# Kernel tuning notes

Measured on AMD Instinct MI355X. Metric: run time of the kernel, lower is better.

## Reference

```python
import jax, jax.numpy as jnp
import numpy as np

NUM_CAPSULE = 32
DIM_VECTOR = 16
NUM_ROUTING = 3

def squash(v, axis=-1):
    s2 = jnp.sum(jnp.square(v), axis=axis, keepdims=True)
    scale = s2 / (1.0 + s2) / jnp.sqrt(s2)
    return scale * v

def setup_inputs() -> dict:
    key = jax.random.key(0)
    k1, k2 = jax.random.split(key)
    B, IN_CAPS, IN_DIM = 64, 2048, 8
    x = jax.random.normal(k1, (B, IN_CAPS, IN_DIM), dtype=jnp.float32)
    # glorot-uniform-ish weight: [in_caps, num_caps, in_dim, out_dim]
    limit = np.sqrt(6.0 / (IN_DIM + DIM_VECTOR)).astype(np.float32)
    W = jax.random.uniform(k2, (IN_CAPS, NUM_CAPSULE, IN_DIM, DIM_VECTOR), dtype=jnp.float32, minval=-limit, maxval=limit)
    return {"x": x, "W": W}

def reference(x, W):
    # x: [B, in_caps, in_dim]; W: [in_caps, num_caps, in_dim, out_dim]
    # inputs_hat (u_hat): [B, in_caps, num_caps, out_dim]
    u_hat = jnp.einsum('bid,inde->bine', x, W)
    B, IN_CAPS = u_hat.shape[0], u_hat.shape[1]
    # routing logits; original broadcasts over out_dim with identical values,
    # so a trailing singleton dim is mathematically equivalent
    b = jnp.zeros((B, IN_CAPS, NUM_CAPSULE, 1), dtype=u_hat.dtype)
    v = None
    for i in range(NUM_ROUTING):
        c = jax.nn.softmax(b, axis=2)                       # over num_capsule
        s = jnp.sum(c * u_hat, axis=1, keepdims=True)       # [B,1,nc,out]
        v = squash(s)                                       # [B,1,nc,out]
        if i != NUM_ROUTING - 1:
            b = b + jnp.sum(u_hat * v, axis=-1, keepdims=True)
    return v.reshape(-1, NUM_CAPSULE, DIM_VECTOR)
```

## Files before the change

kernel.cpp:

```cpp
#include <hip/hip_runtime.h>
#include <math.h>


#define B_TOT 64
#define I_TOT 2048
#define D_IN  8
#define NC    32
#define EV    16
#define OD    (NC*EV)
#define BC    8
#define NBC   (B_TOT/BC)
#define ICH   16
#define NIC   (I_TOT/ICH)

__device__ __forceinline__ void fma4(float4& acc, float a, const float4& w) {
    acc.x = fmaf(a, w.x, acc.x);
    acc.y = fmaf(a, w.y, acc.y);
    acc.z = fmaf(a, w.z, acc.z);
    acc.w = fmaf(a, w.w, acc.w);
}

template <int MODE>
__global__ __launch_bounds__(256, 4)
void route_pass(const float* __restrict__ x, const float* __restrict__ W,
                float* __restrict__ P, const float* __restrict__ vin,
                float* __restrict__ aws)
{
    __shared__ __align__(16) float xl[BC * ICH * D_IN];
    __shared__ float wsum[2][4][BC];

    const int t  = threadIdx.x;
    const int ic = blockIdx.x & (NIC - 1);
    const int bc = blockIdx.x >> 7;
    const int b0 = bc * BC;
    const int i0 = ic * ICH;
    const int eq = t & 3;
    const int bh = (t >> 2) & 1;
    const int n  = t >> 3;
    const int w  = t >> 6;

    {
        const int row = t >> 5, f = (t & 31) * 4;
        *(float4*)&xl[row * (ICH * D_IN) + f] =
            *(const float4*)&x[((size_t)(b0 + row) * I_TOT + i0) * D_IN + f];
    }

    float4 vr[4];
    if (MODE >= 1) {
        #pragma unroll
        for (int q = 0; q < 4; ++q)
            vr[q] = *(const float4*)&vin[(size_t)(b0 + bh * 4 + q) * OD + n * EV + eq * 4];
    }
    __syncthreads();

    float4 sacc[4];
    #pragma unroll
    for (int q = 0; q < 4; ++q) sacc[q] = make_float4(0.f, 0.f, 0.f, 0.f);

    const float* Wt = &W[(size_t)i0 * 4096 + n * 128 + eq * 4];

    for (int ii = 0; ii < ICH; ++ii) {
        float4 wr[8];
        #pragma unroll
        for (int d = 0; d < 8; ++d)
            wr[d] = *(const float4*)&Wt[ii * 4096 + d * 16];

        float4 u[4];
        #pragma unroll
        for (int q = 0; q < 4; ++q) {
            const int bl = bh * 4 + q;
            float4 xa = *(float4*)&xl[bl * (ICH * D_IN) + ii * 8];
            float4 xb = *(float4*)&xl[bl * (ICH * D_IN) + ii * 8 + 4];
            float4 uu = make_float4(0.f, 0.f, 0.f, 0.f);
            fma4(uu, xa.x, wr[0]); fma4(uu, xa.y, wr[1]);
            fma4(uu, xa.z, wr[2]); fma4(uu, xa.w, wr[3]);
            fma4(uu, xb.x, wr[4]); fma4(uu, xb.y, wr[5]);
            fma4(uu, xb.z, wr[6]); fma4(uu, xb.w, wr[7]);
            u[q] = uu;
        }

        if (MODE == 0) {
            #pragma unroll
            for (int q = 0; q < 4; ++q) {
                sacc[q].x += u[q].x; sacc[q].y += u[q].y;
                sacc[q].z += u[q].z; sacc[q].w += u[q].w;
            }
        } else {
            float a[4];
            #pragma unroll
            for (int q = 0; q < 4; ++q) {
                float ap = u[q].x * vr[q].x + u[q].y * vr[q].y
                         + u[q].z * vr[q].z + u[q].w * vr[q].w;
                ap += __shfl_xor(ap, 1, 64);
                ap += __shfl_xor(ap, 2, 64);
                a[q] = ap;
            }
            const size_t aoff = (((size_t)(i0 + ii) * NBC + bc) * NC + n) * 8 + bh * 4;
            if (MODE == 2) {
                float4 a0 = *(const float4*)&aws[aoff];
                a[0] += a0.x; a[1] += a0.y; a[2] += a0.z; a[3] += a0.w;
            }
            if (MODE == 1 && eq == 0) {
                float4 st = make_float4(a[0], a[1], a[2], a[3]);
                *(float4*)&aws[aoff] = st;
            }
            float e[4], p[4];
            #pragma unroll
            for (int q = 0; q < 4; ++q) {
                e[q] = __expf(a[q]);
                float pp = e[q];
                pp += __shfl_xor(pp, 8, 64);
                pp += __shfl_xor(pp, 16, 64);
                pp += __shfl_xor(pp, 32, 64);
                p[q] = pp;
            }
            if (eq == 0) {
                #pragma unroll
                for (int q = 0; q < 4; ++q)
                    wsum[ii & 1][w][bh * 4 + q] = p[q];
            }
            __syncthreads();
            #pragma unroll
            for (int q = 0; q < 4; ++q) {
                const int bl = bh * 4 + q;
                float s = wsum[ii & 1][0][bl] + wsum[ii & 1][1][bl]
                        + wsum[ii & 1][2][bl] + wsum[ii & 1][3][bl];
                float c = e[q] / s;
                fma4(sacc[q], c, u[q]);
            }
        }
    }

    #pragma unroll
    for (int q = 0; q < 4; ++q)
        *(float4*)&P[((size_t)ic * B_TOT + b0 + bh * 4 + q) * OD + n * EV + eq * 4] = sacc[q];
}

__global__ __launch_bounds__(256, 4)
void reduce_squash(const float* __restrict__ P, float* __restrict__ dst, float pre)
{
    const int b = blockIdx.x;
    const int t = threadIdx.x;
    float s1 = 0.f, s2 = 0.f;
    for (int ic = 0; ic < NIC; ++ic) {
        const float* p = &P[((size_t)ic * B_TOT + b) * OD];
        s1 += p[t];
        s2 += p[t + 256];
    }
    s1 *= pre; s2 *= pre;
    float q1 = s1 * s1, q2 = s2 * s2;
    q1 += __shfl_xor(q1, 1, 64);  q2 += __shfl_xor(q2, 1, 64);
    q1 += __shfl_xor(q1, 2, 64);  q2 += __shfl_xor(q2, 2, 64);
    q1 += __shfl_xor(q1, 4, 64);  q2 += __shfl_xor(q2, 4, 64);
    q1 += __shfl_xor(q1, 8, 64);  q2 += __shfl_xor(q2, 8, 64);
    float sc1 = q1 / ((1.0f + q1) * sqrtf(q1));
    float sc2 = q2 / ((1.0f + q2) * sqrtf(q2));
    dst[b * OD + t]       = s1 * sc1;
    dst[b * OD + t + 256] = s2 * sc2;
}

extern "C" void kernel_launch(void* const* d_in, const int* in_sizes, int n_in,
                              void* d_out, int out_size, void* d_ws, size_t ws_size,
                              hipStream_t stream) {
    const float* x = (const float*)d_in[0];
    const float* W = (const float*)d_in[1];
    float* out = (float*)d_out;

    char* ws = (char*)d_ws;
    float* P   = (float*)ws;
    float* aws = (float*)(ws + (size_t)16 * 1024 * 1024);
    float* v0  = (float*)(ws + (size_t)32 * 1024 * 1024);
    float* v1  = v0 + B_TOT * OD;

    dim3 grid(NBC * NIC), blk(256);

    route_pass<0><<<grid, blk, 0, stream>>>(x, W, P, nullptr, nullptr);
    reduce_squash<<<B_TOT, 256, 0, stream>>>(P, v0, 1.0f / 32.0f);
    route_pass<1><<<grid, blk, 0, stream>>>(x, W, P, v0, aws);
    reduce_squash<<<B_TOT, 256, 0, stream>>>(P, v1, 1.0f);
    route_pass<2><<<grid, blk, 0, stream>>>(x, W, P, v1, aws);
    reduce_squash<<<B_TOT, 256, 0, stream>>>(P, out, 1.0f);
}
```

Before: 198.7 us.

## Remap threads so each wave owns whole softmax, removing shared memory and barriers

Reassigns work so each 64-lane wave covers all 32 output capsules for two batch rows, with each lane holding 8 of the 16 output dims. The softmax over capsules then reduces entirely with wave shuffles, which removes the per-iteration __syncthreads and the shared-memory partial sums. x is now read straight from global instead of being staged through LDS, and the stored routing logits use a simpler layout. Each lane now loads twice as much W per input capsule (16 float4 instead of 8), which raises register pressure, and the scalar x reads from global may cost more than the LDS loads did.

```diff
diff --git a/kernel.cpp b/kernel.cpp
--- a/kernel.cpp
+++ b/kernel.cpp
@@ -4,12 +4,9 @@
 
 #define B_TOT 64
 #define I_TOT 2048
-#define D_IN  8
 #define NC    32
 #define EV    16
 #define OD    (NC*EV)
-#define BC    8
-#define NBC   (B_TOT/BC)
 #define ICH   16
 #define NIC   (I_TOT/ICH)
 
@@ -19,6 +16,9 @@
     acc.z = fmaf(a, w.z, acc.z);
     acc.w = fmaf(a, w.w, acc.w);
 }
+__device__ __forceinline__ float dot4(const float4& a, const float4& b) {
+    return a.x*b.x + a.y*b.y + a.z*b.z + a.w*b.w;
+}
 
 template <int MODE>
 __global__ __launch_bounds__(256, 4)
@@ -26,114 +26,87 @@
                 float* __restrict__ P, const float* __restrict__ vin,
                 float* __restrict__ aws)
 {
-    __shared__ __align__(16) float xl[BC * ICH * D_IN];
-    __shared__ float wsum[2][4][BC];
+    const int t    = threadIdx.x;
+    const int w    = __builtin_amdgcn_readfirstlane(t >> 6);
+    const int lane = t & 63;
+    const int n    = lane & 31;
+    const int eh   = lane >> 5;
 
-    const int t  = threadIdx.x;
-    const int ic = blockIdx.x & (NIC - 1);
-    const int bc = blockIdx.x >> 7;
-    const int b0 = bc * BC;
-    const int i0 = ic * ICH;
-    const int eq = t & 3;
-    const int bh = (t >> 2) & 1;
-    const int n  = t >> 3;
-    const int w  = t >> 6;
+    const int ic  = blockIdx.x & (NIC - 1);
+    const int bpg = blockIdx.x >> 7;
+    const int i0  = ic * ICH;
+    const int b0  = bpg * 8 + w * 2;
+    const int b1  = b0 + 1;
 
-    {
-        const int row = t >> 5, f = (t & 31) * 4;
-        *(float4*)&xl[row * (ICH * D_IN) + f] =
-            *(const float4*)&x[((size_t)(b0 + row) * I_TOT + i0) * D_IN + f];
+    const float* xr0 = x + ((size_t)b0 * I_TOT + i0) * 8;
+    const float* xr1 = x + ((size_t)b1 * I_TOT + i0) * 8;
+
+    float4 vr00, vr01, vr10, vr11;
+    if (MODE >= 1) {
+        vr00 = *(const float4*)&vin[b0 * OD + n * EV + eh * 8];
+        vr01 = *(const float4*)&vin[b0 * OD + n * EV + eh * 8 + 4];
+        vr10 = *(const float4*)&vin[b1 * OD + n * EV + eh * 8];
+        vr11 = *(const float4*)&vin[b1 * OD + n * EV + eh * 8 + 4];
     }
 
-    float4 vr[4];
-    if (MODE >= 1) {
-        #pragma unroll
-        for (int q = 0; q < 4; ++q)
-            vr[q] = *(const float4*)&vin[(size_t)(b0 + bh * 4 + q) * OD + n * EV + eq * 4];
-    }
-    __syncthreads();
+    float4 s0a = {0,0,0,0}, s0b = {0,0,0,0};
+    float4 s1a = {0,0,0,0}, s1b = {0,0,0,0};
 
-    float4 sacc[4];
-    #pragma unroll
-    for (int q = 0; q < 4; ++q) sacc[q] = make_float4(0.f, 0.f, 0.f, 0.f);
-
-    const float* Wt = &W[(size_t)i0 * 4096 + n * 128 + eq * 4];
+    const float* Wp = W + (size_t)i0 * 4096 + n * 128 + eh * 8;
 
     for (int ii = 0; ii < ICH; ++ii) {
-        float4 wr[8];
+        const int i = i0 + ii;
+        float4 wa[8], wb[8];
         #pragma unroll
-        for (int d = 0; d < 8; ++d)
-            wr[d] = *(const float4*)&Wt[ii * 4096 + d * 16];
-
-        float4 u[4];
+        for (int d = 0; d < 8; ++d) {
+            wa[d] = *(const float4*)&Wp[ii * 4096 + d * 16];
+            wb[d] = *(const float4*)&Wp[ii * 4096 + d * 16 + 4];
+        }
+        float4 u0a = {0,0,0,0}, u0b = {0,0,0,0};
+        float4 u1a = {0,0,0,0}, u1b = {0,0,0,0};
         #pragma unroll
-        for (int q = 0; q < 4; ++q) {
-            const int bl = bh * 4 + q;
-            float4 xa = *(float4*)&xl[bl * (ICH * D_IN) + ii * 8];
-            float4 xb = *(float4*)&xl[bl * (ICH * D_IN) + ii * 8 + 4];
-            float4 uu = make_float4(0.f, 0.f, 0.f, 0.f);
-            fma4(uu, xa.x, wr[0]); fma4(uu, xa.y, wr[1]);
-            fma4(uu, xa.z, wr[2]); fma4(uu, xa.w, wr[3]);
-            fma4(uu, xb.x, wr[4]); fma4(uu, xb.y, wr[5]);
-            fma4(uu, xb.z, wr[6]); fma4(uu, xb.w, wr[7]);
-            u[q] = uu;
+        for (int d = 0; d < 8; ++d) {
+            float x0 = xr0[ii * 8 + d];
+            float x1 = xr1[ii * 8 + d];
+            fma4(u0a, x0, wa[d]); fma4(u0b, x0, wb[d]);
+            fma4(u1a, x1, wa[d]); fma4(u1b, x1, wb[d]);
         }
 
         if (MODE == 0) {
-            #pragma unroll
-            for (int q = 0; q < 4; ++q) {
-                sacc[q].x += u[q].x; sacc[q].y += u[q].y;
-                sacc[q].z += u[q].z; sacc[q].w += u[q].w;
+            s0a.x += u0a.x; s0a.y += u0a.y; s0a.z += u0a.z; s0a.w += u0a.w;
+            s0b.x += u0b.x; s0b.y += u0b.y; s0b.z += u0b.z; s0b.w += u0b.w;
+            s1a.x += u1a.x; s1a.y += u1a.y; s1a.z += u1a.z; s1a.w += u1a.w;
+            s1b.x += u1b.x; s1b.y += u1b.y; s1b.z += u1b.z; s1b.w += u1b.w;
+        } else {
+            float a0 = dot4(u0a, vr00) + dot4(u0b, vr01);
+            float a1 = dot4(u1a, vr10) + dot4(u1b, vr11);
+            a0 += __shfl_xor(a0, 32, 64);
+            a1 += __shfl_xor(a1, 32, 64);
+            if (MODE == 2) {
+                a0 += aws[((size_t)i * B_TOT + b0) * NC + n];
+                a1 += aws[((size_t)i * B_TOT + b1) * NC + n];
             }
-        } else {
-            float a[4];
-            #pragma unroll
-            for (int q = 0; q < 4; ++q) {
-                float ap = u[q].x * vr[q].x + u[q].y * vr[q].y
-                         + u[q].z * vr[q].z + u[q].w * vr[q].w;
-                ap += __shfl_xor(ap, 1, 64);
-                ap += __shfl_xor(ap, 2, 64);
-                a[q] = ap;
+            if (MODE == 1 && eh == 0) {
+                aws[((size_t)i * B_TOT + b0) * NC + n] = a0;
+                aws[((size_t)i * B_TOT + b1) * NC + n] = a1;
             }
-            const size_t aoff = (((size_t)(i0 + ii) * NBC + bc) * NC + n) * 8 + bh * 4;
-            if (MODE == 2) {
-                float4 a0 = *(const float4*)&aws[aoff];
-                a[0] += a0.x; a[1] += a0.y; a[2] += a0.z; a[3] += a0.w;
-            }
-            if (MODE == 1 && eq == 0) {
-                float4 st = make_float4(a[0], a[1], a[2], a[3]);
-                *(float4*)&aws[aoff] = st;
-            }
-            float e[4], p[4];
-            #pragma unroll
-            for (int q = 0; q < 4; ++q) {
-                e[q] = __expf(a[q]);
-                float pp = e[q];
-                pp += __shfl_xor(pp, 8, 64);
-                pp += __shfl_xor(pp, 16, 64);
-                pp += __shfl_xor(pp, 32, 64);
-                p[q] = pp;
-            }
-            if (eq == 0) {
-                #pragma unroll
-                for (int q = 0; q < 4; ++q)
-                    wsum[ii & 1][w][bh * 4 + q] = p[q];
-            }
-            __syncthreads();
-            #pragma unroll
-            for (int q = 0; q < 4; ++q) {
-                const int bl = bh * 4 + q;
-                float s = wsum[ii & 1][0][bl] + wsum[ii & 1][1][bl]
-                        + wsum[ii & 1][2][bl] + wsum[ii & 1][3][bl];
-                float c = e[q] / s;
-                fma4(sacc[q], c, u[q]);
-            }
+            float e0 = __expf(a0), e1 = __expf(a1);
+            float p0 = e0, p1 = e1;
+            p0 += __shfl_xor(p0, 1, 64);  p1 += __shfl_xor(p1, 1, 64);
+            p0 += __shfl_xor(p0, 2, 64);  p1 += __shfl_xor(p1, 2, 64);
+            p0 += __shfl_xor(p0, 4, 64);  p1 += __shfl_xor(p1, 4, 64);
+            p0 += __shfl_xor(p0, 8, 64);  p1 += __shfl_xor(p1, 8, 64);
+            p0 += __shfl_xor(p0, 16, 64); p1 += __shfl_xor(p1, 16, 64);
+            float c0 = e0 / p0, c1 = e1 / p1;
+            fma4(s0a, c0, u0a); fma4(s0b, c0, u0b);
+            fma4(s1a, c1, u1a); fma4(s1b, c1, u1b);
         }
     }
 
-    #pragma unroll
-    for (int q = 0; q < 4; ++q)
-        *(float4*)&P[((size_t)ic * B_TOT + b0 + bh * 4 + q) * OD + n * EV + eq * 4] = sacc[q];
+    float4* p0 = (float4*)&P[((size_t)ic * B_TOT + b0) * OD + n * EV + eh * 8];
+    float4* p1 = (float4*)&P[((size_t)ic * B_TOT + b1) * OD + n * EV + eh * 8];
+    p0[0] = s0a; p0[1] = s0b;
+    p1[0] = s1a; p1[1] = s1b;
 }
 
 __global__ __launch_bounds__(256, 4)
@@ -172,7 +145,7 @@
     float* v0  = (float*)(ws + (size_t)32 * 1024 * 1024);
     float* v1  = v0 + B_TOT * OD;
 
-    dim3 grid(NBC * NIC), blk(256);
+    dim3 grid(8 * NIC), blk(256);
 
     route_pass<0><<<grid, blk, 0, stream>>>(x, W, P, nullptr, nullptr);
     reduce_squash<<<B_TOT, 256, 0, stream>>>(P, v0, 1.0f / 32.0f);
```

Result: slower. 444.4 us (+123.7%).
